# Performance work log

Measured on AMD Instinct MI355X. Metric: run time of the kernel, lower is better.

Reference implementation:

```python
import jax, jax.numpy as jnp
import numpy as np

HEAD_NUM = 16
EMBED = 1024

def setup_inputs() -> dict:
    key = jax.random.key(0)
    k1, k2, k3 = jax.random.split(key, 3)
    x = jax.random.normal(k1, (2, 2048, EMBED), dtype=jnp.float32)
    W_qkv = jax.random.normal(k2, (3 * EMBED, EMBED), dtype=jnp.float32) * (EMBED ** -0.5)
    W_out = jax.random.normal(k3, (EMBED, EMBED), dtype=jnp.float32) * (EMBED ** -0.5)
    return {"x": x, "W_qkv": W_qkv, "W_out": W_out}

def reference(x, W_qkv, W_out):
    b, t, E = x.shape
    h = HEAD_NUM
    d = E // h
    dk = (E / h) ** 0.5
    qkv = x @ W_qkv.T  # [b, t, 3E]
    # einops 'b t (d k h) -> k b h t d' with k=3, h=head_num (d outermost in the split)
    qkv = qkv.reshape(b, t, d, 3, h).transpose(3, 0, 4, 1, 2)  # [3, b, h, t, d]
    q, k, v = qkv[0], qkv[1], qkv[2]
    energy = jnp.einsum('bhid,bhjd->bhij', q, k) / dk  # [b, h, t, t]
    attn = jax.nn.softmax(energy, axis=-1)
    out = jnp.einsum('bhij,bhjd->bhid', attn, v)  # [b, h, t, d]
    out = out.transpose(0, 2, 1, 3).reshape(b, t, E)  # 'b h t d -> b t (h d)'
    return out @ W_out.T
```

## Files before the change

### kernel.cpp

```cpp
#include <hip/hip_runtime.h>
#include <hip/hip_bf16.h>


#define HEADS 16
#define EMB   1024
#define HDIM  64
#define BB    2
#define TT    2048
#define QSCALE 0.18033688011112042f

typedef __attribute__((ext_vector_type(8)))  short      bf16x8;
typedef __attribute__((ext_vector_type(8)))  _Float16   f16x8;
typedef __attribute__((ext_vector_type(4)))  float      f32x4;
typedef __attribute__((ext_vector_type(16))) float      f32x16;
typedef __attribute__((ext_vector_type(4)))  unsigned   u32x4;

__device__ __forceinline__ unsigned short f2bf(float f) {
    __hip_bfloat16 h = __float2bfloat16(f);
    return __builtin_bit_cast(unsigned short, h);
}
__device__ __forceinline__ float fexp2(float x) {
#if __has_builtin(__builtin_amdgcn_exp2f)
    return __builtin_amdgcn_exp2f(x);
#else
    return exp2f(x);
#endif
}
__device__ __forceinline__ unsigned pkrtz(float a, float b) {
    auto r = __builtin_amdgcn_cvt_pkrtz(a, b);
    return __builtin_bit_cast(unsigned, r);
}
__device__ __forceinline__ unsigned short f2h(float f) {
    return (unsigned short)(pkrtz(f, 0.f) & 0xffffu);
}
__device__ __forceinline__ float h2f(unsigned short u) {
    return (float)__builtin_bit_cast(_Float16, u);
}
__device__ __forceinline__ void gload_lds16(const void* g, void* l) {
    __builtin_amdgcn_global_load_lds(
        (const __attribute__((address_space(1))) void*)g,
        (__attribute__((address_space(3))) void*)l, 16, 0, 0);
}
__device__ __forceinline__ int swzi(int row, int blk) {
    return row * 64 + ((blk ^ (row & 7)) << 3);
}
__device__ __forceinline__ void pl32swap(unsigned& a, unsigned& b) {
    asm("v_permlane32_swap_b32 %0, %1" : "+v"(a), "+v"(b));
}

__global__ __launch_bounds__(256)
void conv_bf16(const float* __restrict__ src, unsigned short* __restrict__ dst,
               int n8) {
    int i = blockIdx.x * 256 + threadIdx.x;
    if (i >= n8) return;
    const float4 v0 = ((const float4*)src)[i * 2];
    const float4 v1 = ((const float4*)src)[i * 2 + 1];
    ushort4 a, b;
    a.x = f2bf(v0.x); a.y = f2bf(v0.y); a.z = f2bf(v0.z); a.w = f2bf(v0.w);
    b.x = f2bf(v1.x); b.y = f2bf(v1.y); b.z = f2bf(v1.z); b.w = f2bf(v1.w);
    ((ushort4*)dst)[i * 2]     = a;
    ((ushort4*)dst)[i * 2 + 1] = b;
}

template<int PERM>
__global__ __launch_bounds__(256)
void convw(const float* __restrict__ src, unsigned short* __restrict__ dst) {
    const int np = blockIdx.x;
    const int ns = PERM ? ((np & 63) * 48 + (np >> 10) * 16 + ((np >> 6) & 15))
                        : np;
    const float4 v = ((const float4*)(src + (size_t)ns * 1024))[threadIdx.x];
    ushort4 u;
    u.x = f2bf(v.x); u.y = f2bf(v.y); u.z = f2bf(v.z); u.w = f2bf(v.w);
    ((ushort4*)(dst + (size_t)np * 1024))[threadIdx.x] = u;
}

template<int EPI>
__global__ __launch_bounds__(256)
void gemm_bf16(const unsigned short* __restrict__ Ag,
               const unsigned short* __restrict__ Wg,
               float* __restrict__ Cout,
               unsigned short* __restrict__ QKb,
               unsigned short* __restrict__ Vt) {
    __shared__ __align__(16) unsigned short Ab[128 * 64];
    __shared__ __align__(16) unsigned short Wb[128 * 64];

    const int tid = threadIdx.x, lane = tid & 63, w = tid >> 6;
    const int n0 = blockIdx.x * 128, m0 = blockIdx.y * 128;
    const int wn = (w >> 1) * 64, wm = (w & 1) * 64;
    const int r16 = lane & 15, g = lane >> 4;

    f32x4 acc[4][4];
    #pragma unroll
    for (int i = 0; i < 4; ++i)
        #pragma unroll
        for (int j = 0; j < 4; ++j)
            acc[i][j] = (f32x4){0.f, 0.f, 0.f, 0.f};

    const int srl = lane >> 3;
    const int scb = lane & 7;

    for (int kt = 0; kt < 16; ++kt) {
        __syncthreads();
        const int k0 = kt * 64;
        #pragma unroll
        for (int i = 0; i < 4; ++i) {
            const int row = w * 32 + i * 8 + srl;
            const int cbs = (scb ^ (row & 7)) << 3;
            gload_lds16(Ag + (size_t)(m0 + row) * 1024 + k0 + cbs,
                        Ab + (size_t)(w * 32 + i * 8) * 64);
            gload_lds16(Wg + (size_t)(n0 + row) * 1024 + k0 + cbs,
                        Wb + (size_t)(w * 32 + i * 8) * 64);
        }
        __syncthreads();

        #pragma unroll
        for (int ks = 0; ks < 2; ++ks) {
            bf16x8 xf[4];
            #pragma unroll
            for (int mi = 0; mi < 4; ++mi)
                xf[mi] = *(const bf16x8*)&Ab[swzi(wm + mi * 16 + r16, ks * 4 + g)];
            #pragma unroll
            for (int ni = 0; ni < 4; ++ni) {
                const bf16x8 wf = *(const bf16x8*)&Wb[swzi(wn + ni * 16 + r16, ks * 4 + g)];
                #pragma unroll
                for (int mi = 0; mi < 4; ++mi)
                    acc[ni][mi] = __builtin_amdgcn_mfma_f32_16x16x32_bf16(
                        wf, xf[mi], acc[ni][mi], 0, 0, 0);
            }
        }
    }

    const int gq = g * 4;
    if (EPI == 0) {
        #pragma unroll
        for (int ni = 0; ni < 4; ++ni)
            #pragma unroll
            for (int mi = 0; mi < 4; ++mi) {
                const int m = m0 + wm + mi * 16 + r16;
                *(f32x4*)&Cout[(size_t)m * 1024 + (n0 + wn + ni * 16 + gq)] =
                    acc[ni][mi];
            }
    } else if (n0 < 2048) {
        #pragma unroll
        for (int ni = 0; ni < 4; ++ni) {
            const float qs = (n0 + wn + ni * 16) < 1024 ? QSCALE : 1.0f;
            #pragma unroll
            for (int mi = 0; mi < 4; ++mi) {
                const int m  = m0 + wm + mi * 16 + r16;
                const int np = n0 + wn + ni * 16 + gq;
                ushort4 u;
                u.x = f2bf(acc[ni][mi][0] * qs); u.y = f2bf(acc[ni][mi][1] * qs);
                u.z = f2bf(acc[ni][mi][2] * qs); u.w = f2bf(acc[ni][mi][3] * qs);
                *(ushort4*)&QKb[(size_t)m * 2048 + np] = u;
            }
        }
    } else {
        const int b = m0 >> 11, t0 = m0 & 2047;
        #pragma unroll
        for (int ni = 0; ni < 4; ++ni)
            #pragma unroll
            for (int mi = 0; mi < 4; ++mi) {
                const int t   = t0 + wm + mi * 16 + r16;
                const int nv0 = (n0 - 2048) + wn + ni * 16 + gq;
                #pragma unroll
                for (int j = 0; j < 4; ++j) {
                    const int nv = nv0 + j, h = nv >> 6, d = nv & 63;
                    Vt[(((size_t)(b * HEADS + h)) * HDIM + d) * TT + t] =
                        f2h(acc[ni][mi][j]);
                }
            }
    }
}

__global__ __launch_bounds__(256, 4)
void attn32(const unsigned short* __restrict__ QKb,
            const unsigned short* __restrict__ Vt,
            unsigned short* __restrict__ PO0,
            unsigned short* __restrict__ PO1,
            float* __restrict__ PL0,
            float* __restrict__ PL1) {
    __shared__ __align__(16) unsigned short Ks[2][64 * 64];
    __shared__ __align__(16) unsigned short Vs[2][64 * 64];

    const int tid = threadIdx.x, lane = tid & 63, w = tid >> 6;
    const int l31 = lane & 31, hi = lane >> 5;
    const int qt = blockIdx.x & 15, kh = blockIdx.x >> 4;
    const int h = blockIdx.y, b = blockIdx.z;
    const int kbase = kh * 1024;
    const unsigned short* Vsrc = Vt + (size_t)(b * HEADS + h) * HDIM * TT;
    unsigned short* PO = kh ? PO1 : PO0;
    float*          PL = kh ? PL1 : PL0;

    bf16x8 qf[4];
    {
        const unsigned short* qrow =
            QKb + ((size_t)(b * TT + qt * 128 + w * 32 + l31)) * 2048 + h * HDIM;
        #pragma unroll
        for (int dc = 0; dc < 4; ++dc)
            qf[dc] = *(const bf16x8*)(qrow + dc * 16 + hi * 8);
    }

    const f32x16 zz = {};
    f32x16 o0 = {}, o1 = {};
    float lrun = 0.f;

    const int srl = lane >> 3;
    const int scb = lane & 7;
    const int cbs = (scb ^ srl) << 3;
    const int rl0 = w * 16 + srl, rl1 = rl0 + 8;
    const unsigned short* kp0 =
        QKb + (size_t)(b * TT + kbase + rl0) * 2048 + 1024 + h * HDIM + cbs;
    const unsigned short* kp1 = kp0 + (size_t)8 * 2048;
    const unsigned short* vp0 = Vsrc + (size_t)rl0 * TT + kbase + cbs;
    const unsigned short* vp1 = vp0 + (size_t)8 * TT;
    unsigned short* const kd0 = &Ks[0][(w * 16) * 64];
    unsigned short* const kd1 = &Ks[1][(w * 16) * 64];
    unsigned short* const vd0 = &Vs[0][(w * 16) * 64];
    unsigned short* const vd1 = &Vs[1][(w * 16) * 64];

#define STAGE(KD, VD)                                                  \
    do {                                                               \
        gload_lds16(kp0, (KD));        gload_lds16(kp1, (KD) + 512);   \
        gload_lds16(vp0, (VD));        gload_lds16(vp1, (VD) + 512);   \
        kp0 += 64 * 2048; kp1 += 64 * 2048; vp0 += 64; vp1 += 64;      \
    } while (0)

    STAGE(kd0, vd0);

    for (int jt = 0; jt < 16; ++jt) {
        const int bb = jt & 1;
        __syncthreads();
        if (jt < 15) {
            if (bb) STAGE(kd0, vd0); else STAGE(kd1, vd1);
        }
        const unsigned short* KsB = &Ks[bb][0];
        const unsigned short* VsB = &Vs[bb][0];

        f32x16 stA, stB;
        __builtin_amdgcn_s_setprio(1);
        #pragma unroll
        for (int dc = 0; dc < 4; ++dc) {
            const bf16x8 kaA = *(const bf16x8*)&KsB[swzi(l31,      dc * 2 + hi)];
            const bf16x8 kaB = *(const bf16x8*)&KsB[swzi(32 + l31, dc * 2 + hi)];
            if (dc == 0) {
                stA = __builtin_amdgcn_mfma_f32_32x32x16_bf16(kaA, qf[0], zz, 0, 0, 0);
                stB = __builtin_amdgcn_mfma_f32_32x32x16_bf16(kaB, qf[0], zz, 0, 0, 0);
            } else {
                stA = __builtin_amdgcn_mfma_f32_32x32x16_bf16(kaA, qf[dc], stA, 0, 0, 0);
                stB = __builtin_amdgcn_mfma_f32_32x32x16_bf16(kaB, qf[dc], stB, 0, 0, 0);
            }
        }
        __builtin_amdgcn_s_setprio(0);

        #pragma unroll
        for (int x = 0; x < 2; ++x) {
            const f32x16& st = x ? stB : stA;
            float sum;
            unsigned wd[8];
            #pragma unroll
            for (int c = 0; c < 4; ++c) {
                const float e0 = fexp2(st[4 * c + 0]);
                const float e1 = fexp2(st[4 * c + 1]);
                const float e2 = fexp2(st[4 * c + 2]);
                const float e3 = fexp2(st[4 * c + 3]);
                const float s4 = (e0 + e1) + (e2 + e3);
                sum = c ? sum + s4 : s4;
                wd[2 * c]     = pkrtz(e0, e1);
                wd[2 * c + 1] = pkrtz(e2, e3);
            }
            lrun += sum;

            unsigned a0 = wd[0], a2 = wd[2];  pl32swap(a0, a2);
            unsigned a1 = wd[1], a3 = wd[3];  pl32swap(a1, a3);
            unsigned b0 = wd[4], b2 = wd[6];  pl32swap(b0, b2);
            unsigned b1 = wd[5], b3 = wd[7];  pl32swap(b1, b3);
            const u32x4 fa = {a0, a1, a2, a3};
            const u32x4 fb = {b0, b1, b2, b3};
            const f16x8 pa0 = __builtin_bit_cast(f16x8, fa);
            const f16x8 pa1 = __builtin_bit_cast(f16x8, fb);

            const int f0 = 2 * x;
            __builtin_amdgcn_s_setprio(1);
            {
                const f16x8 vb00 = *(const f16x8*)&VsB[swzi(l31,      f0 * 2 + hi)];
                const f16x8 vb01 = *(const f16x8*)&VsB[swzi(32 + l31, f0 * 2 + hi)];
                o0 = __builtin_amdgcn_mfma_f32_32x32x16_f16(pa0, vb00, o0, 0, 0, 0);
                o1 = __builtin_amdgcn_mfma_f32_32x32x16_f16(pa0, vb01, o1, 0, 0, 0);
                const f16x8 vb10 = *(const f16x8*)&VsB[swzi(l31,      (f0 + 1) * 2 + hi)];
                const f16x8 vb11 = *(const f16x8*)&VsB[swzi(32 + l31, (f0 + 1) * 2 + hi)];
                o0 = __builtin_amdgcn_mfma_f32_32x32x16_f16(pa1, vb10, o0, 0, 0, 0);
                o1 = __builtin_amdgcn_mfma_f32_32x32x16_f16(pa1, vb11, o1, 0, 0, 0);
            }
            __builtin_amdgcn_s_setprio(0);
        }
    }
#undef STAGE

    lrun += __shfl_xor(lrun, 32);
    const float inv = 1.0f / lrun;
    #pragma unroll
    for (int r = 0; r < 16; ++r) {
        const int qr = (r & 3) + 8 * (r >> 2) + 4 * hi;
        const float ir = __shfl(inv, qr);
        const int q = qt * 128 + w * 32 + qr;
        unsigned short* dst = PO + ((size_t)(b * TT + q)) * EMB + h * HDIM + l31;
        dst[0]  = f2h(o0[r] * ir);
        dst[32] = f2h(o1[r] * ir);
    }
    if (!hi) {
        const int q = qt * 128 + w * 32 + l31;
        PL[((size_t)(b * HEADS + h)) * TT + q] = lrun;
    }
}

__global__ __launch_bounds__(256)
void merge_attn(const unsigned short* __restrict__ PO0,
                const unsigned short* __restrict__ PO1,
                const float* __restrict__ PL0,
                const float* __restrict__ PL1,
                unsigned short* __restrict__ AOb) {
    const int i = blockIdx.x * 256 + threadIdx.x;
    const int tg  = i >> 8;
    const int col = (i & 255) * 4;
    const int h   = col >> 6;
    const int b   = tg >> 11, t = tg & 2047;

    const float la = PL0[((size_t)(b * HEADS + h)) * TT + t];
    const float lb = PL1[((size_t)(b * HEADS + h)) * TT + t];
    const float inv = 1.0f / (la + lb);
    const float wa = la * inv, wb = lb * inv;

    const ushort4 a = ((const ushort4*)PO0)[i];
    const ushort4 c = ((const ushort4*)PO1)[i];
    ushort4 o;
    o.x = f2bf(h2f(a.x) * wa + h2f(c.x) * wb);
    o.y = f2bf(h2f(a.y) * wa + h2f(c.y) * wb);
    o.z = f2bf(h2f(a.z) * wa + h2f(c.z) * wb);
    o.w = f2bf(h2f(a.w) * wa + h2f(c.w) * wb);
    ((ushort4*)AOb)[i] = o;
}

extern "C" void kernel_launch(void* const* d_in, const int* in_sizes, int n_in,
                              void* d_out, int out_size, void* d_ws, size_t ws_size,
                              hipStream_t stream) {
    const float* x    = (const float*)d_in[0];
    const float* Wqkv = (const float*)d_in[1];
    const float* Wout = (const float*)d_in[2];
    float* out = (float*)d_out;

    unsigned short* Wqb = (unsigned short*)d_ws;
    unsigned short* Wob = Wqb + 3145728;
    unsigned short* xb  = Wob + 1048576;
    unsigned short* QKb = xb  + 4194304;
    unsigned short* Vt  = QKb + 8388608;
    unsigned short* PO0 = Vt  + 4194304;
    unsigned short* PO1 = PO0 + 4194304;
    float*          PL0 = (float*)(PO1 + 4194304);
    float*          PL1 = PL0 + 65536;
    unsigned short* AOb = xb;

    conv_bf16<<<2048, 256, 0, stream>>>(x, xb, 524288);
    convw<1><<<3072, 256, 0, stream>>>(Wqkv, Wqb);
    convw<0><<<1024, 256, 0, stream>>>(Wout, Wob);

    gemm_bf16<1><<<dim3(24, 32), 256, 0, stream>>>(xb, Wqb, nullptr, QKb, Vt);

    attn32<<<dim3(32, 16, 2), 256, 0, stream>>>(QKb, Vt, PO0, PO1, PL0, PL1);

    merge_attn<<<4096, 256, 0, stream>>>(PO0, PO1, PL0, PL1, AOb);

    gemm_bf16<0><<<dim3(8, 32), 256, 0, stream>>>(AOb, Wob, out, nullptr, nullptr);
}
```

Before: 134.3 us.

## Triple-buffer GEMM K-tiles with async LDS prefetch and single barrier

Replaces the GEMM's single-buffered 64-wide K loop, which had two barriers per step, with a three-stage ring of 32-wide K tiles. Loads for step kt+2 are issued while step kt computes, using vmcnt waits and one barrier per iteration. It adds a new XOR swizzle for the narrower tiles and raises wave priority around the MFMA block. The goal is to hide global-to-LDS load latency behind the matrix math, at the cost of twice as many loop iterations and somewhat more LDS.

```diff
diff --git a/kernel.cpp b/kernel.cpp
--- a/kernel.cpp
+++ b/kernel.cpp
@@ -81,13 +81,14 @@
                float* __restrict__ Cout,
                unsigned short* __restrict__ QKb,
                unsigned short* __restrict__ Vt) {
-    __shared__ __align__(16) unsigned short Ab[128 * 64];
-    __shared__ __align__(16) unsigned short Wb[128 * 64];
+    __shared__ __align__(16) unsigned short AbL[3][128 * 32];
+    __shared__ __align__(16) unsigned short WbL[3][128 * 32];
 
     const int tid = threadIdx.x, lane = tid & 63, w = tid >> 6;
     const int n0 = blockIdx.x * 128, m0 = blockIdx.y * 128;
     const int wn = (w >> 1) * 64, wm = (w & 1) * 64;
     const int r16 = lane & 15, g = lane >> 4;
+    const int goff = ((g ^ ((r16 >> 1) & 3)) << 3);
 
     f32x4 acc[4][4];
     #pragma unroll
@@ -96,39 +97,52 @@
         for (int j = 0; j < 4; ++j)
             acc[i][j] = (f32x4){0.f, 0.f, 0.f, 0.f};
 
-    const int srl = lane >> 3;
-    const int scb = lane & 7;
-
-    for (int kt = 0; kt < 16; ++kt) {
-        __syncthreads();
-        const int k0 = kt * 64;
-        #pragma unroll
-        for (int i = 0; i < 4; ++i) {
-            const int row = w * 32 + i * 8 + srl;
-            const int cbs = (scb ^ (row & 7)) << 3;
-            gload_lds16(Ag + (size_t)(m0 + row) * 1024 + k0 + cbs,
-                        Ab + (size_t)(w * 32 + i * 8) * 64);
-            gload_lds16(Wg + (size_t)(n0 + row) * 1024 + k0 + cbs,
-                        Wb + (size_t)(w * 32 + i * 8) * 64);
-        }
-        __syncthreads();
-
-        #pragma unroll
-        for (int ks = 0; ks < 2; ++ks) {
-            bf16x8 xf[4];
+    const int srow = w * 16 + (lane >> 2);
+    const int scol = ((lane & 3) ^ ((lane >> 3) & 3)) << 3;
+    const int sdst = (w * 16) * 32;
+    const unsigned short* Asrc = Ag + (size_t)(m0 + srow) * 1024 + scol;
+    const unsigned short* Wsrc = Wg + (size_t)(n0 + srow) * 1024 + scol;
+
+#define STAGE(AB, WB, K0)                                            \
+    do {                                                             \
+        gload_lds16(Asrc + (K0),              (AB) + sdst);          \
+        gload_lds16(Asrc + (K0) + 64 * 1024,  (AB) + sdst + 2048);   \
+        gload_lds16(Wsrc + (K0),              (WB) + sdst);          \
+        gload_lds16(Wsrc + (K0) + 64 * 1024,  (WB) + sdst + 2048);   \
+    } while (0)
+
+    unsigned short *pa0 = &AbL[0][0], *pa1 = &AbL[1][0], *pa2 = &AbL[2][0];
+    unsigned short *pw0 = &WbL[0][0], *pw1 = &WbL[1][0], *pw2 = &WbL[2][0];
+
+    STAGE(pa0, pw0, 0);
+    STAGE(pa1, pw1, 32);
+
+    for (int kt = 0; kt < 32; ++kt) {
+        if (kt < 31) asm volatile("s_waitcnt vmcnt(4)" ::: "memory");
+        else         asm volatile("s_waitcnt vmcnt(0)" ::: "memory");
+        __builtin_amdgcn_s_barrier();
+        if (kt < 30) STAGE(pa2, pw2, (kt + 2) * 32);
+
+        bf16x8 xf[4];
+        #pragma unroll
+        for (int mi = 0; mi < 4; ++mi)
+            xf[mi] = *(const bf16x8*)&pa0[(wm + mi * 16 + r16) * 32 + goff];
+        __builtin_amdgcn_s_setprio(1);
+        #pragma unroll
+        for (int ni = 0; ni < 4; ++ni) {
+            const bf16x8 wf = *(const bf16x8*)&pw0[(wn + ni * 16 + r16) * 32 + goff];
             #pragma unroll
             for (int mi = 0; mi < 4; ++mi)
-                xf[mi] = *(const bf16x8*)&Ab[swzi(wm + mi * 16 + r16, ks * 4 + g)];
-            #pragma unroll
-            for (int ni = 0; ni < 4; ++ni) {
-                const bf16x8 wf = *(const bf16x8*)&Wb[swzi(wn + ni * 16 + r16, ks * 4 + g)];
-                #pragma unroll
-                for (int mi = 0; mi < 4; ++mi)
-                    acc[ni][mi] = __builtin_amdgcn_mfma_f32_16x16x32_bf16(
-                        wf, xf[mi], acc[ni][mi], 0, 0, 0);
-            }
-        }
-    }
+                acc[ni][mi] = __builtin_amdgcn_mfma_f32_16x16x32_bf16(
+                    wf, xf[mi], acc[ni][mi], 0, 0, 0);
+        }
+        __builtin_amdgcn_s_setprio(0);
+
+        unsigned short* t;
+        t = pa0; pa0 = pa1; pa1 = pa2; pa2 = t;
+        t = pw0; pw0 = pw1; pw1 = pw2; pw2 = t;
+    }
+#undef STAGE
 
     const int gq = g * 4;
     if (EPI == 0) {
@@ -207,7 +221,7 @@
     const int srl = lane >> 3;
     const int scb = lane & 7;
     const int cbs = (scb ^ srl) << 3;
-    const int rl0 = w * 16 + srl, rl1 = rl0 + 8;
+    const int rl0 = w * 16 + srl;
     const unsigned short* kp0 =
         QKb + (size_t)(b * TT + kbase + rl0) * 2048 + 1024 + h * HDIM + cbs;
     const unsigned short* kp1 = kp0 + (size_t)8 * 2048;
```

After: 135.2 us. About the same (+0.6%).
